# Kernel tuning notes

Measured on AMD Instinct MI355X. Metric: run time of the kernel, lower is better.

## Reference

```python
import jax, jax.numpy as jnp
import numpy as np

DIMS = [11, 20, 20, 30, 30, 40, 40, 40, 20, 10, 1]  # layer widths

def setup_inputs() -> dict:
    key = jax.random.key(0)
    ks = jax.random.split(key, 1 + 2 * (len(DIMS) - 1))
    inp = {"x": jax.random.normal(ks[0], (2000000, 11), dtype=jnp.float32)}
    for i in range(len(DIMS) - 1):
        d_in, d_out = DIMS[i], DIMS[i + 1]
        bound = 1.0 / np.sqrt(d_in)
        inp[f"W{i}"] = jax.random.uniform(ks[1 + 2 * i], (d_out, d_in), dtype=jnp.float32, minval=-bound, maxval=bound)
        inp[f"b{i}"] = jax.random.uniform(ks[2 + 2 * i], (d_out,), dtype=jnp.float32, minval=-bound, maxval=bound)
    return inp

def _swish(x):
    return x * jax.nn.sigmoid(x)

def reference(x, W0, b0, W1, b1, W2, b2, W3, b3, W4, b4, W5, b5, W6, b6, W7, b7, W8, b8, W9, b9):
    Ws = [W0, W1, W2, W3, W4, W5, W6, W7, W8, W9]
    bs = [b0, b1, b2, b3, b4, b5, b6, b7, b8, b9]
    h = x
    for i in range(9):  # 9 Linear+Swish blocks
        h = _swish(h @ Ws[i].T + bs[i])
    h = jax.nn.relu(h @ Ws[9].T + bs[9])  # final Linear(10,1) + ReLU
    return h.reshape(-1)
```

## Files before the change

kernel.cpp:

```cpp
#include <hip/hip_runtime.h>
#include <math.h>


typedef _Float16 half8 __attribute__((ext_vector_type(8)));
typedef _Float16 half4 __attribute__((ext_vector_type(4)));
typedef _Float16 half2 __attribute__((ext_vector_type(2)));
typedef float f32x4 __attribute__((ext_vector_type(4)));

__device__ __forceinline__ int swz(int a) {
    return a ^ (((a >> 7) & 1) << 4) ^ (((a >> 8) & 1) << 5);
}

__device__ __forceinline__ float swish_f(float a) {
    float e = __expf(-a);
    return a * __builtin_amdgcn_rcpf(1.0f + e);
}

__device__ __forceinline__ half4 pack4(const float (&v)[4]) {
    auto lo = __builtin_amdgcn_cvt_pkrtz(v[0], v[1]);
    auto hi = __builtin_amdgcn_cvt_pkrtz(v[2], v[3]);
    union {
        half4 h4;
        half2 h2[2];
    } u;
    u.h2[0] = __builtin_bit_cast(half2, lo);
    u.h2[1] = __builtin_bit_cast(half2, hi);
    return u.h4;
}

__device__ __forceinline__ half8 make_frag32(const float* __restrict__ W,
                                             const float* __restrict__ b,
                                             int IN, int OUT, int ot, int lr,
                                             int kg) {
    const int r = ot * 16 + lr;
    half8 h;
#pragma unroll
    for (int e = 0; e < 8; ++e) {
        const int k = kg * 8 + e;
        float v = 0.0f;
        if (r < OUT) {
            if (k < IN)
                v = W[r * IN + k];
            else if (k == IN)
                v = b[r];
        }
        h[e] = (_Float16)v;
    }
    return h;
}

__device__ __forceinline__ half4 make_frag16(const float* __restrict__ W,
                                             const float* __restrict__ b,
                                             int IN, int OUT, int ot, int kb,
                                             int lr, int kg) {
    const int r = ot * 16 + lr;
    half4 h;
#pragma unroll
    for (int e = 0; e < 4; ++e) {
        const int k = kb + kg * 4 + e;
        float v = 0.0f;
        if (r < OUT) {
            if (k < IN)
                v = W[r * IN + k];
            else if (k == IN)
                v = b[r];
        }
        h[e] = (_Float16)v;
    }
    return h;
}

struct TP {
    const half8* r0;
    const half4* r1;
    _Float16* w0;
    _Float16* w1;
    _Float16* wk;
};

template <int NK0, int MARK, int NOT>
__device__ __forceinline__ void epi_kt0(const f32x4 (&A)[NOT], const TP& t,
                                        int kg) {
#pragma unroll
    for (int ot = 0; ot < NK0; ++ot) {
        float v[4];
#pragma unroll
        for (int r = 0; r < 4; ++r) {
            v[r] = swish_f(A[ot][r]);
            if (ot == MARK / 16 && ot * 16 + kg * 4 + r == MARK) v[r] = 1.0f;
        }
        _Float16* wp = (ot == 0) ? t.w0 : t.w1;
        *(half4*)wp = pack4(v);
    }
}

template <int MREL>
__device__ __forceinline__ void epi_kt1(const f32x4& a, const TP& t, int kg) {
    float v[4];
#pragma unroll
    for (int r = 0; r < 4; ++r) {
        v[r] = swish_f(a[r]);
        if constexpr (MREL >= 0) {
            if (kg * 4 + r == MREL) v[r] = 1.0f;
        }
    }
    *(half4*)t.wk = pack4(v);
}

template <int NOT, bool K1>
__device__ __forceinline__ void compute2(const _Float16* __restrict__ w32,
                                         const _Float16* __restrict__ w16,
                                         const TP& t0, const TP& t1,
                                         f32x4 (&A)[NOT], f32x4 (&B)[NOT],
                                         int lane) {
    const f32x4 z4 = {0.f, 0.f, 0.f, 0.f};
    const half8 b0 = *t0.r0;
    const half8 b1 = *t1.r0;
#pragma unroll
    for (int ot = 0; ot < NOT; ++ot) {
        const half8 wf = *(const half8*)(w32 + ot * 512 + lane * 8);
        A[ot] = __builtin_amdgcn_mfma_f32_16x16x32_f16(wf, b0, z4, 0, 0, 0);
        B[ot] = __builtin_amdgcn_mfma_f32_16x16x32_f16(wf, b1, z4, 0, 0, 0);
    }
    if constexpr (K1) {
        const half4 c0 = *t0.r1;
        const half4 c1 = *t1.r1;
#pragma unroll
        for (int ot = 0; ot < NOT; ++ot) {
            const half4 wg = *(const half4*)(w16 + ot * 256 + lane * 4);
            A[ot] = __builtin_amdgcn_mfma_f32_16x16x16f16(wg, c0, A[ot], 0, 0, 0);
            B[ot] = __builtin_amdgcn_mfma_f32_16x16x16f16(wg, c1, B[ot], 0, 0, 0);
        }
    }
}

template <int NOT, bool K1, int NK0, int MARK, int MREL>
__device__ __forceinline__ void layerX(const _Float16* __restrict__ w32,
                                       const _Float16* __restrict__ w16,
                                       const TP& t0, const TP& t1, int lane,
                                       int kg) {
    f32x4 A[NOT], B[NOT];
    compute2<NOT, K1>(w32, w16, t0, t1, A, B, lane);
    epi_kt0<NK0, MARK>(A, t0, kg);
    epi_kt0<NK0, MARK>(B, t1, kg);
    if constexpr (NOT > NK0) {
        epi_kt1<MREL>(A[NK0], t0, kg);
        epi_kt1<MREL>(B[NK0], t1, kg);
    }
}

__device__ __forceinline__ half4 load_x4(const float* __restrict__ x,
                                         int row0, int lr, int kg) {
    half4 b = {};
    const float* xr = x + (size_t)(row0 + lr) * 11;
#pragma unroll
    for (int e = 0; e < 4; ++e) {
        const int k = kg * 4 + e;
        float v = (k < 11) ? xr[k] : ((k == 11) ? 1.0f : 0.0f);
        b[e] = (_Float16)v;
    }
    return b;
}

__global__ __launch_bounds__(256, 4) void longnet_mlp_r9(
    const float* __restrict__ x,
    const float* __restrict__ W0, const float* __restrict__ b0,
    const float* __restrict__ W1, const float* __restrict__ b1,
    const float* __restrict__ W2, const float* __restrict__ b2,
    const float* __restrict__ W3, const float* __restrict__ b3,
    const float* __restrict__ W4, const float* __restrict__ b4,
    const float* __restrict__ W5, const float* __restrict__ b5,
    const float* __restrict__ W6, const float* __restrict__ b6,
    const float* __restrict__ W7, const float* __restrict__ b7,
    const float* __restrict__ W8, const float* __restrict__ b8,
    const float* __restrict__ W9, const float* __restrict__ b9,
    float* __restrict__ out, int n) {
    __shared__ __align__(16) _Float16 s_w[12032];
    __shared__ __align__(16) _Float16 s_act[6144];

    const int tid = threadIdx.x;
    const int lane = tid & 63;
    const int wave = tid >> 6;
    const int lr = lane & 15;
    const int kg = lane >> 4;
    const int kgl = kg & 1;
    const int kgh = kg >> 1;

    _Float16* const s_w16 = s_w + 9216;

    {
        const float* Wt[10] = {W0, W1, W2, W3, W4, W5, W6, W7, W8, W9};
        const float* bt[10] = {b0, b1, b2, b3, b4, b5, b6, b7, b8, b9};
        const int INs[10] = {11, 20, 20, 30, 30, 40, 40, 40, 20, 10};
        const int OUTs[10] = {20, 20, 30, 30, 40, 40, 40, 20, 10, 1};
        const int L32[18] = {1, 1, 2, 2, 3, 3, 4, 4, 4, 5, 5, 5, 6, 6, 6, 7, 7, 8};
        const int O32[18] = {0, 1, 0, 1, 0, 1, 0, 1, 2, 0, 1, 2, 0, 1, 2, 0, 1, 0};
#pragma unroll
        for (int i = 0; i < 18; ++i)
            if ((i & 3) == wave) {
                const int L = L32[i];
                half8 h = make_frag32(Wt[L], bt[L], INs[L], OUTs[L], O32[i],
                                      lr, kg);
                *(half8*)(s_w + i * 512 + lane * 8) = h;
            }
        const int L16[11] = {0, 0, 5, 5, 5, 6, 6, 6, 7, 7, 9};
        const int O16[11] = {0, 1, 0, 1, 2, 0, 1, 2, 0, 1, 0};
        const int KB16[11] = {0, 0, 32, 32, 32, 32, 32, 32, 32, 32, 0};
#pragma unroll
        for (int i = 0; i < 11; ++i)
            if (((18 + i) & 3) == wave) {
                const int L = L16[i];
                half4 h = make_frag16(Wt[L], bt[L], INs[L], OUTs[L], O16[i],
                                      KB16[i], lr, kg);
                *(half4*)(s_w16 + i * 256 + lane * 4) = h;
            }
    }

    char* const c0 = (char*)s_act + wave * 3072;
    char* const c1 = c0 + 1536;
    const int rd0 = swz(lane * 16);
    const int rk1 = 1024 + lane * 8;
    const int wo0 = swz((kgh & 3) * 256 + lr * 16 + kgl * 8);
    const int wo1 = swz(((2 + kgh) & 3) * 256 + lr * 16 + kgl * 8);
    const TP t0 = {(const half8*)(c0 + rd0), (const half4*)(c0 + rk1),
                   (_Float16*)(c0 + wo0), (_Float16*)(c0 + wo1),
                   (_Float16*)(c0 + rk1)};
    const TP t1 = {(const half8*)(c1 + rd0), (const half4*)(c1 + rk1),
                   (_Float16*)(c1 + wo0), (_Float16*)(c1 + wo1),
                   (_Float16*)(c1 + rk1)};

    {
        int* a32 = (int*)c0;
#pragma unroll
        for (int i = 0; i < 12; ++i) a32[i * 64 + lane] = 0;
    }
    __syncthreads();

    const f32x4 z4 = {0.f, 0.f, 0.f, 0.f};
    const int npair = n >> 5;
    const int step = (int)gridDim.x * 4;

    for (int t = blockIdx.x * 4 + wave; t < npair; t += step) {
        const int row0 = t * 32;

        {
            const half4 xb0 = load_x4(x, row0, lr, kg);
            const half4 xb1 = load_x4(x, row0 + 16, lr, kg);
            f32x4 A[2], B[2];
#pragma unroll
            for (int ot = 0; ot < 2; ++ot) {
                const half4 wg = *(const half4*)(s_w16 + ot * 256 + lane * 4);
                A[ot] = __builtin_amdgcn_mfma_f32_16x16x16f16(wg, xb0, z4, 0, 0, 0);
                B[ot] = __builtin_amdgcn_mfma_f32_16x16x16f16(wg, xb1, z4, 0, 0, 0);
            }
            epi_kt0<2, 20>(A, t0, kg);
            epi_kt0<2, 20>(B, t1, kg);
        }
        layerX<2, false, 2, 20, -1>(s_w + 0 * 512, s_w, t0, t1, lane, kg);
        layerX<2, false, 2, 30, -1>(s_w + 2 * 512, s_w, t0, t1, lane, kg);
        layerX<2, false, 2, 30, -1>(s_w + 4 * 512, s_w, t0, t1, lane, kg);
        layerX<3, false, 2, 1000, 8>(s_w + 6 * 512, s_w, t0, t1, lane, kg);
        layerX<3, true, 2, 1000, 8>(s_w + 9 * 512, s_w16 + 2 * 256, t0, t1, lane, kg);
        layerX<3, true, 2, 1000, 8>(s_w + 12 * 512, s_w16 + 5 * 256, t0, t1, lane, kg);
        layerX<2, true, 2, 20, -1>(s_w + 15 * 512, s_w16 + 8 * 256, t0, t1, lane, kg);
        layerX<1, false, 0, 1000, 10>(s_w + 17 * 512, s_w, t0, t1, lane, kg);

        {
            const half4 wg = *(const half4*)(s_w16 + 10 * 256 + lane * 4);
            f32x4 F0 = __builtin_amdgcn_mfma_f32_16x16x16f16(wg, *t0.r1, z4, 0, 0, 0);
            f32x4 F1 = __builtin_amdgcn_mfma_f32_16x16x16f16(wg, *t1.r1, z4, 0, 0, 0);
            if (kg == 0) {
                out[row0 + lr] = fmaxf(F0[0], 0.0f);
                out[row0 + 16 + lr] = fmaxf(F1[0], 0.0f);
            }
        }
    }
}

extern "C" void kernel_launch(void* const* d_in, const int* in_sizes, int n_in,
                              void* d_out, int out_size, void* d_ws, size_t ws_size,
                              hipStream_t stream) {
    const float* x = (const float*)d_in[0];
    const float* W0 = (const float*)d_in[1];
    const float* b0 = (const float*)d_in[2];
    const float* W1 = (const float*)d_in[3];
    const float* b1 = (const float*)d_in[4];
    const float* W2 = (const float*)d_in[5];
    const float* b2 = (const float*)d_in[6];
    const float* W3 = (const float*)d_in[7];
    const float* b3 = (const float*)d_in[8];
    const float* W4 = (const float*)d_in[9];
    const float* b4 = (const float*)d_in[10];
    const float* W5 = (const float*)d_in[11];
    const float* b5 = (const float*)d_in[12];
    const float* W6 = (const float*)d_in[13];
    const float* b6 = (const float*)d_in[14];
    const float* W7 = (const float*)d_in[15];
    const float* b7 = (const float*)d_in[16];
    const float* W8 = (const float*)d_in[17];
    const float* b8 = (const float*)d_in[18];
    const float* W9 = (const float*)d_in[19];
    const float* b9 = (const float*)d_in[20];
    float* out = (float*)d_out;

    const int n = in_sizes[0] / 11;
    const int grid = 1024;

    longnet_mlp_r9<<<grid, 256, 0, stream>>>(
        x, W0, b0, W1, b1, W2, b2, W3, b3, W4, b4, W5, b5, W6, b6, W7, b7, W8,
        b8, W9, b9, out, n);
}
```

Before: 179.6 us.

## Pre-pack fp16 weight fragments in a prep kernel and read them from global

Adds a one-block prep kernel that packs the weight and bias MFMA fragments into a workspace buffer. The main kernel then reads weights from global/L2 instead of building them in LDS, which drops the per-block fragment construction, the __syncthreads and about 24KB of LDS per block. Occupancy bounds go from 4 to 8 blocks, with a 2048-block grid. The cost is an extra kernel launch, and the hot loop now does weight loads through the cache hierarchy rather than from LDS.

Measured after the change: 276.5 us. 1.54x slower.

```diff
diff --git a/kernel.cpp b/kernel.cpp
--- a/kernel.cpp
+++ b/kernel.cpp
@@ -68,6 +68,57 @@
         h[e] = (_Float16)v;
     }
     return h;
+}
+
+#define FRAG_TABLES                                                           \
+    const float* Wt[10] = {W0, W1, W2, W3, W4, W5, W6, W7, W8, W9};           \
+    const float* bt[10] = {b0, b1, b2, b3, b4, b5, b6, b7, b8, b9};           \
+    const int INs[10] = {11, 20, 20, 30, 30, 40, 40, 40, 20, 10};             \
+    const int OUTs[10] = {20, 20, 30, 30, 40, 40, 40, 20, 10, 1};             \
+    const int L32[18] = {1, 1, 2, 2, 3, 3, 4, 4, 4,                           \
+                         5, 5, 5, 6, 6, 6, 7, 7, 8};                          \
+    const int O32[18] = {0, 1, 0, 1, 0, 1, 0, 1, 2,                           \
+                         0, 1, 2, 0, 1, 2, 0, 1, 0};                          \
+    const int L16[11] = {0, 0, 5, 5, 5, 6, 6, 6, 7, 7, 9};                    \
+    const int O16[11] = {0, 1, 0, 1, 2, 0, 1, 2, 0, 1, 0};                    \
+    const int KB16[11] = {0, 0, 32, 32, 32, 32, 32, 32, 32, 32, 0};
+
+#define WPARAMS                                                               \
+    const float *__restrict__ W0, const float *__restrict__ b0,               \
+        const float *__restrict__ W1, const float *__restrict__ b1,           \
+        const float *__restrict__ W2, const float *__restrict__ b2,           \
+        const float *__restrict__ W3, const float *__restrict__ b3,           \
+        const float *__restrict__ W4, const float *__restrict__ b4,           \
+        const float *__restrict__ W5, const float *__restrict__ b5,           \
+        const float *__restrict__ W6, const float *__restrict__ b6,           \
+        const float *__restrict__ W7, const float *__restrict__ b7,           \
+        const float *__restrict__ W8, const float *__restrict__ b8,           \
+        const float *__restrict__ W9, const float *__restrict__ b9
+
+__global__ __launch_bounds__(256) void longnet_prep(WPARAMS,
+                                                    _Float16* __restrict__ gw) {
+    const int tid = threadIdx.x;
+    const int lane = tid & 63;
+    const int wave = tid >> 6;
+    const int lr = lane & 15;
+    const int kg = lane >> 4;
+    _Float16* const gw16 = gw + 9216;
+    FRAG_TABLES
+#pragma unroll
+    for (int i = 0; i < 18; ++i)
+        if ((i & 3) == wave) {
+            const int L = L32[i];
+            half8 h = make_frag32(Wt[L], bt[L], INs[L], OUTs[L], O32[i], lr, kg);
+            *(half8*)(gw + i * 512 + lane * 8) = h;
+        }
+#pragma unroll
+    for (int i = 0; i < 11; ++i)
+        if (((18 + i) & 3) == wave) {
+            const int L = L16[i];
+            half4 h = make_frag16(Wt[L], bt[L], INs[L], OUTs[L], O16[i],
+                                  KB16[i], lr, kg);
+            *(half4*)(gw16 + i * 256 + lane * 4) = h;
+        }
 }
 
 struct TP {
@@ -162,21 +213,12 @@
     return b;
 }
 
-__global__ __launch_bounds__(256, 4) void longnet_mlp_r9(
-    const float* __restrict__ x,
-    const float* __restrict__ W0, const float* __restrict__ b0,
-    const float* __restrict__ W1, const float* __restrict__ b1,
-    const float* __restrict__ W2, const float* __restrict__ b2,
-    const float* __restrict__ W3, const float* __restrict__ b3,
-    const float* __restrict__ W4, const float* __restrict__ b4,
-    const float* __restrict__ W5, const float* __restrict__ b5,
-    const float* __restrict__ W6, const float* __restrict__ b6,
-    const float* __restrict__ W7, const float* __restrict__ b7,
-    const float* __restrict__ W8, const float* __restrict__ b8,
-    const float* __restrict__ W9, const float* __restrict__ b9,
+template <bool GW, int MINW>
+__global__ __launch_bounds__(256, MINW) void longnet_mlp_r10(
+    const float* __restrict__ x, WPARAMS, const _Float16* __restrict__ gw,
     float* __restrict__ out, int n) {
-    __shared__ __align__(16) _Float16 s_w[12032];
     __shared__ __align__(16) _Float16 s_act[6144];
+    __shared__ __align__(16) _Float16 s_w[GW ? 8 : 12032];
 
     const int tid = threadIdx.x;
     const int lane = tid & 63;
@@ -186,15 +228,11 @@
     const int kgl = kg & 1;
     const int kgh = kg >> 1;
 
-    _Float16* const s_w16 = s_w + 9216;
-
-    {
-        const float* Wt[10] = {W0, W1, W2, W3, W4, W5, W6, W7, W8, W9};
-        const float* bt[10] = {b0, b1, b2, b3, b4, b5, b6, b7, b8, b9};
-        const int INs[10] = {11, 20, 20, 30, 30, 40, 40, 40, 20, 10};
-        const int OUTs[10] = {20, 20, 30, 30, 40, 40, 40, 20, 10, 1};
-        const int L32[18] = {1, 1, 2, 2, 3, 3, 4, 4, 4, 5, 5, 5, 6, 6, 6, 7, 7, 8};
-        const int O32[18] = {0, 1, 0, 1, 0, 1, 0, 1, 2, 0, 1, 2, 0, 1, 2, 0, 1, 0};
+    const _Float16* wb;
+    if constexpr (GW) {
+        wb = gw;
+    } else {
+        FRAG_TABLES
 #pragma unroll
         for (int i = 0; i < 18; ++i)
             if ((i & 3) == wave) {
@@ -203,18 +241,17 @@
                                       lr, kg);
                 *(half8*)(s_w + i * 512 + lane * 8) = h;
             }
-        const int L16[11] = {0, 0, 5, 5, 5, 6, 6, 6, 7, 7, 9};
-        const int O16[11] = {0, 1, 0, 1, 2, 0, 1, 2, 0, 1, 0};
-        const int KB16[11] = {0, 0, 32, 32, 32, 32, 32, 32, 32, 32, 0};
 #pragma unroll
         for (int i = 0; i < 11; ++i)
             if (((18 + i) & 3) == wave) {
                 const int L = L16[i];
                 half4 h = make_frag16(Wt[L], bt[L], INs[L], OUTs[L], O16[i],
                                       KB16[i], lr, kg);
-                *(half4*)(s_w16 + i * 256 + lane * 4) = h;
+                *(half4*)(s_w + 9216 + i * 256 + lane * 4) = h;
             }
-    }
+        wb = s_w;
+    }
+    const _Float16* const w16 = wb + 9216;
 
     char* const c0 = (char*)s_act + wave * 3072;
     char* const c1 = c0 + 1536;
@@ -234,7 +271,7 @@
 #pragma unroll
         for (int i = 0; i < 12; ++i) a32[i * 64 + lane] = 0;
     }
-    __syncthreads();
+    if constexpr (!GW) __syncthreads();
 
     const f32x4 z4 = {0.f, 0.f, 0.f, 0.f};
     const int npair = n >> 5;
@@ -249,24 +286,24 @@
             f32x4 A[2], B[2];
 #pragma unroll
             for (int ot = 0; ot < 2; ++ot) {
-                const half4 wg = *(const half4*)(s_w16 + ot * 256 + lane * 4);
+                const half4 wg = *(const half4*)(w16 + ot * 256 + lane * 4);
                 A[ot] = __builtin_amdgcn_mfma_f32_16x16x16f16(wg, xb0, z4, 0, 0, 0);
                 B[ot] = __builtin_amdgcn_mfma_f32_16x16x16f16(wg, xb1, z4, 0, 0, 0);
             }
             epi_kt0<2, 20>(A, t0, kg);
             epi_kt0<2, 20>(B, t1, kg);
         }
-        layerX<2, false, 2, 20, -1>(s_w + 0 * 512, s_w, t0, t1, lane, kg);
-        layerX<2, false, 2, 30, -1>(s_w + 2 * 512, s_w, t0, t1, lane, kg);
-        layerX<2, false, 2, 30, -1>(s_w + 4 * 512, s_w, t0, t1, lane, kg);
-        layerX<3, false, 2, 1000, 8>(s_w + 6 * 512, s_w, t0, t1, lane, kg);
-        layerX<3, true, 2, 1000, 8>(s_w + 9 * 512, s_w16 + 2 * 256, t0, t1, lane, kg);
-        layerX<3, true, 2, 1000, 8>(s_w + 12 * 512, s_w16 + 5 * 256, t0, t1, lane, kg);
-        layerX<2, true, 2, 20, -1>(s_w + 15 * 512, s_w16 + 8 * 256, t0, t1, lane, kg);
-        layerX<1, false, 0, 1000, 10>(s_w + 17 * 512, s_w, t0, t1, lane, kg);
+        layerX<2, false, 2, 20, -1>(wb + 0 * 512, w16, t0, t1, lane, kg);
+        layerX<2, false, 2, 30, -1>(wb + 2 * 512, w16, t0, t1, lane, kg);
+        layerX<2, false, 2, 30, -1>(wb + 4 * 512, w16, t0, t1, lane, kg);
+        layerX<3, false, 2, 1000, 8>(wb + 6 * 512, w16, t0, t1, lane, kg);
+        layerX<3, true, 2, 1000, 8>(wb + 9 * 512, w16 + 2 * 256, t0, t1, lane, kg);
+        layerX<3, true, 2, 1000, 8>(wb + 12 * 512, w16 + 5 * 256, t0, t1, lane, kg);
+        layerX<2, true, 2, 20, -1>(wb + 15 * 512, w16 + 8 * 256, t0, t1, lane, kg);
+        layerX<1, false, 0, 1000, 10>(wb + 17 * 512, w16, t0, t1, lane, kg);
 
         {
-            const half4 wg = *(const half4*)(s_w16 + 10 * 256 + lane * 4);
+            const half4 wg = *(const half4*)(w16 + 10 * 256 + lane * 4);
             f32x4 F0 = __builtin_amdgcn_mfma_f32_16x16x16f16(wg, *t0.r1, z4, 0, 0, 0);
             f32x4 F1 = __builtin_amdgcn_mfma_f32_16x16x16f16(wg, *t1.r1, z4, 0, 0, 0);
             if (kg == 0) {
@@ -304,9 +341,19 @@
     float* out = (float*)d_out;
 
     const int n = in_sizes[0] / 11;
-    const int grid = 1024;
-
-    longnet_mlp_r9<<<grid, 256, 0, stream>>>(
-        x, W0, b0, W1, b1, W2, b2, W3, b3, W4, b4, W5, b5, W6, b6, W7, b7, W8,
-        b8, W9, b9, out, n);
-}
+    const size_t WBYTES = 12032 * sizeof(_Float16);
+
+    if (ws_size >= WBYTES) {
+        _Float16* gw = (_Float16*)d_ws;
+        longnet_prep<<<1, 256, 0, stream>>>(
+            W0, b0, W1, b1, W2, b2, W3, b3, W4, b4, W5, b5, W6, b6, W7, b7,
+            W8, b8, W9, b9, gw);
+        longnet_mlp_r10<true, 8><<<2048, 256, 0, stream>>>(
+            x, W0, b0, W1, b1, W2, b2, W3, b3, W4, b4, W5, b5, W6, b6, W7, b7,
+            W8, b8, W9, b9, gw, out, n);
+    } else {
+        longnet_mlp_r10<false, 4><<<1024, 256, 0, stream>>>(
+            x, W0, b0, W1, b1, W2, b2, W3, b3, W4, b4, W5, b5, W6, b6, W7, b7,
+            W8, b8, W9, b9, nullptr, out, n);
+    }
+}
```
